# Kernel optimization log

Measured on AMD Instinct MI355X. Metric: run time of the kernel, lower is better.

## Reference

```python
import jax, jax.numpy as jnp
import numpy as np

B, N, D = 64, 128, 32
P = N * (N - 1)          # ordered pairs
H1, H2, HF = 32, 32, 16  # layer_widths=(32,32), final_widths=(16,)
EPS = 1e-5
SLOPE = 0.01             # LeakyReLU default


def _leaky(x):
    return jnp.where(x >= 0, x, SLOPE * x)


def setup_inputs() -> dict:
    key = jax.random.key(0)
    ks = jax.random.split(key, 16)
    # all ordered pairs (i, j), i != j, grouped by source i
    src = np.repeat(np.arange(N), N - 1)
    tgt = np.array([j for i in range(N) for j in range(N) if j != i])
    s = 0.1
    return {
        "inputs": jax.random.normal(ks[0], (B, N, D), jnp.float32),
        "src": jnp.asarray(src, jnp.int32),
        "tgt": jnp.asarray(tgt, jnp.int32),
        # edge MLP: Linear(2D,32) -> BN1d(P) -> LeakyReLU -> Linear(32,32) -> LeakyReLU -> Linear(32, 1+D)
        "W1": jax.random.normal(ks[1], (2 * D, H1), jnp.float32) * s,
        "b1": jnp.zeros((H1,), jnp.float32),
        "g1": jnp.ones((P,), jnp.float32),
        "be1": jnp.zeros((P,), jnp.float32),
        "W2": jax.random.normal(ks[2], (H1, H2), jnp.float32) * s,
        "b2": jnp.zeros((H2,), jnp.float32),
        "W3": jax.random.normal(ks[3], (H2, 1 + D), jnp.float32) * s,
        "b3": jnp.zeros((1 + D,), jnp.float32),
        # final MLP: Linear(2D,16) -> BN1d(16) -> LeakyReLU -> Linear(16, D)
        "Wf1": jax.random.normal(ks[4], (2 * D, HF), jnp.float32) * s,
        "bf1": jnp.zeros((HF,), jnp.float32),
        "gf": jnp.ones((HF,), jnp.float32),
        "bef": jnp.zeros((HF,), jnp.float32),
        "Wf2": jax.random.normal(ks[5], (HF, D), jnp.float32) * s,
        "bf2": jnp.zeros((D,), jnp.float32),
    }


def reference(inputs, src, tgt, W1, b1, g1, be1, W2, b2, W3, b3,
              Wf1, bf1, gf, bef, Wf2, bf2):
    b, n, d = inputs.shape
    # gather pair features: (B, P, 2D)
    paired = jnp.concatenate([inputs[:, src], inputs[:, tgt]], axis=2)
    h = paired @ W1 + b1                              # (B, P, H1)
    # BatchNorm1d(P) on (B, P, H1): normalize per pair channel over (batch, feat)
    m = h.mean(axis=(0, 2), keepdims=True)
    v = h.var(axis=(0, 2), keepdims=True)
    h = (h - m) * jax.lax.rsqrt(v + EPS) * g1[None, :, None] + be1[None, :, None]
    h = _leaky(h) @ W2 + b2
    h = _leaky(h) @ W3 + b3                           # (B, P, 1+D)
    edges = jax.nn.sigmoid(h[..., :1])                # (B, P, 1)
    messages = h[..., 1:]                             # (B, P, D)
    weighted = edges * messages
    # segment-sum over the (N-1) senders per source node
    agg = weighted.reshape(b, n, n - 1, d).sum(axis=2)  # (B, N, D)
    sm = jnp.concatenate([inputs, agg], axis=2).reshape(-1, 2 * d)
    f = sm @ Wf1 + bf1                                # (B*N, HF)
    mf = f.mean(axis=0)
    vf = f.var(axis=0)
    f = (f - mf) * jax.lax.rsqrt(vf + EPS) * gf + bef
    out = _leaky(f) @ Wf2 + bf2
    return edges[..., 0], out.reshape(b, n, d)
```

## Files before the change

kernel.cpp:

```cpp
#include <hip/hip_runtime.h>
#include <hip/hip_bf16.h>
#include <math.h>

#define BB 64
#define NN 128
#define DD 32
#define PP (NN * (NN - 1))
#define EPSF 1e-5f

typedef __attribute__((ext_vector_type(8))) short bf16x8;
typedef __attribute__((ext_vector_type(4))) float f32x4;

static __device__ __forceinline__ unsigned short f2bf(float x) {
    unsigned u = __builtin_bit_cast(unsigned, x);
    u += 0x7fff + ((u >> 16) & 1);
    return (unsigned short)(u >> 16);
}
static __device__ __forceinline__ unsigned pk2bf(float a, float b) {
    return (unsigned)f2bf(a) | ((unsigned)f2bf(b) << 16);
}
static __device__ __forceinline__ float leakyf(float x) {
    return fmaxf(x, 0.01f * x);
}

__global__ __launch_bounds__(256) void proj_kernel(
    const float* __restrict__ inputs, const float* __restrict__ W1,
    const float* __restrict__ b1,
    const float* __restrict__ W2, const float* __restrict__ W3,
    float* __restrict__ AT, float* __restrict__ BT,
    unsigned short* __restrict__ ATh, unsigned short* __restrict__ BTh,
    float* __restrict__ SA, float* __restrict__ QA,
    float* __restrict__ SB, float* __restrict__ QB,
    unsigned short* __restrict__ W2p, unsigned short* __restrict__ W3p,
    float* __restrict__ fpartA, float* __restrict__ fpartB)
{
    __shared__ float Xs[64][33];
    __shared__ float W1s[64][32];
    __shared__ float red[4][4];

    int n = blockIdx.x, tid = threadIdx.x;

    for (int idx = tid; idx < 2048; idx += 256) {
        int b = idx >> 5, d = idx & 31;
        Xs[b][d] = inputs[((size_t)b << 12) + ((size_t)n << 5) + d];
        W1s[idx >> 5][idx & 31] = W1[idx];
    }
    __syncthreads();

    int j = tid & 31, rb = tid >> 5;
    float b1j = b1[j];
    float sa = 0.f, qa = 0.f, sb = 0.f, qb = 0.f;
    #pragma unroll
    for (int i = 0; i < 8; ++i) {
        int b = rb * 8 + i;
        float a = b1j, c = 0.f;
        #pragma unroll
        for (int k = 0; k < 32; ++k) {
            a += Xs[b][k] * W1s[k][j];
            c += Xs[b][k] * W1s[32 + k][j];
        }
        size_t off = ((size_t)n * 64 + b) * 32 + j;
        AT[off] = a;  BT[off] = c;
        ATh[off] = f2bf(a);  BTh[off] = f2bf(c);
        sa += a; qa += a * a; sb += c; qb += c * c;
    }
    #pragma unroll
    for (int off = 32; off > 0; off >>= 1) {
        sa += __shfl_down(sa, off, 64);
        qa += __shfl_down(qa, off, 64);
        sb += __shfl_down(sb, off, 64);
        qb += __shfl_down(qb, off, 64);
    }
    int w = tid >> 6;
    if ((tid & 63) == 0) { red[w][0] = sa; red[w][1] = qa; red[w][2] = sb; red[w][3] = qb; }
    __syncthreads();
    if (tid == 0) {
        SA[n] = red[0][0] + red[1][0] + red[2][0] + red[3][0];
        QA[n] = red[0][1] + red[1][1] + red[2][1] + red[3][1];
        SB[n] = red[0][2] + red[1][2] + red[2][2] + red[3][2];
        QB[n] = red[0][3] + red[1][3] + red[2][3] + red[3][3];
    }

    if (blockIdx.x == 0 && tid < 64) {
        int l = tid, nn2 = l & 15, kc = l >> 4;
        #pragma unroll
        for (int ct = 0; ct < 2; ++ct)
            #pragma unroll
            for (int jj = 0; jj < 8; ++jj) {
                int k = kc * 8 + jj;
                W2p[(ct * 64 + l) * 8 + jj] = f2bf(W2[k * 32 + ct * 16 + nn2]);
            }
        #pragma unroll
        for (int ct = 0; ct < 3; ++ct)
            #pragma unroll
            for (int jj = 0; jj < 8; ++jj) {
                int k = kc * 8 + jj;
                int c = ct * 16 + nn2;
                W3p[(ct * 64 + l) * 8 + jj] = f2bf(c < 33 ? W3[k * 33 + c] : 0.f);
            }
    }
    if (blockIdx.x == 1) {
        for (int idx = tid; idx < 1024; idx += 256) {
            fpartA[idx] = 0.f;
            fpartB[idx] = 0.f;
        }
    }
}

__global__ __launch_bounds__(256) void stats2_kernel(
    const unsigned short* __restrict__ ATh, const unsigned short* __restrict__ BTh,
    const float* __restrict__ SA, const float* __restrict__ QA,
    const float* __restrict__ SB, const float* __restrict__ QB,
    const float* __restrict__ g1, const float* __restrict__ be1,
    float* __restrict__ statA, float* __restrict__ statB)
{
    __shared__ __align__(16) float part[4][64][4];
    int tid = threadIdx.x;
    int lane = tid & 63, w = tid >> 6;
    int s0 = (blockIdx.x >> 3) * 16, t0 = (blockIdx.x & 7) * 16;

    int m = lane & 15, kc = lane >> 4;
    const unsigned short* abase = ATh + (size_t)(s0 + m) * 2048 + kc * 8 + w * 512;
    const unsigned short* bbase = BTh + (size_t)(t0 + m) * 2048 + kc * 8 + w * 512;

    f32x4 acc = {0.f, 0.f, 0.f, 0.f};
    #pragma unroll
    for (int step = 0; step < 16; ++step) {
        bf16x8 av = *(const bf16x8*)(abase + step * 32);
        bf16x8 bv = *(const bf16x8*)(bbase + step * 32);
        acc = __builtin_amdgcn_mfma_f32_16x16x32_bf16(av, bv, acc, 0, 0, 0);
    }
    *(f32x4*)&part[w][lane][0] = acc;
    __syncthreads();

    if (w == 0) {
        #pragma unroll
        for (int ww = 1; ww < 4; ++ww) {
            f32x4 o = *(const f32x4*)&part[ww][lane][0];
            acc[0] += o[0]; acc[1] += o[1]; acc[2] += o[2]; acc[3] += o[3];
        }
        int col = lane & 15, quad = lane >> 4;
        int t = t0 + col;
        float sbt = SB[t], qbt = QB[t];
        #pragma unroll
        for (int r = 0; r < 4; ++r) {
            int s = s0 + quad * 4 + r;
            if (s != t) {
                int e = t - (t > s);
                int p = s * 127 + e;
                float S = SA[s] + sbt;
                float Q = QA[s] + qbt + 2.f * acc[r];
                float mean = S * (1.f / 2048.f);
                float var  = Q * (1.f / 2048.f) - mean * mean;
                float inv  = rsqrtf(var + EPSF);
                float sc   = inv * g1[p];
                statA[p] = sc;
                statB[p] = be1[p] - mean * sc;
            }
        }
    }
}

__global__ __launch_bounds__(256) void edges_kernel(
    const float* __restrict__ AT, const float* __restrict__ BT,
    const float* __restrict__ statA, const float* __restrict__ statB,
    const unsigned short* __restrict__ W2p, const unsigned short* __restrict__ W3p,
    const float* __restrict__ b2, const float* __restrict__ b3,
    const float* __restrict__ inputs, const float* __restrict__ Wf1,
    const float* __restrict__ bf1,
    float* __restrict__ edges_out, float* __restrict__ agg,
    float* __restrict__ f, float* __restrict__ fpartA, float* __restrict__ fpartB)
{
    __shared__ __align__(16) unsigned short Abuf[8][64][8];
    __shared__ __align__(16) unsigned short Hbuf[8][64][8];
    __shared__ __align__(16) float evb[128];
    __shared__ float aggbuf[32];

    int tid = threadIdx.x;
    int b = blockIdx.x >> 7;
    int s = blockIdx.x & 127;

    if (tid < 32) aggbuf[tid] = 0.f;

    int e2 = tid >> 1;
    int half = tid & 1;
    int k0 = half * 16;
    int m = e2 & 15, r = e2 >> 4;
    const float* arow = AT + ((size_t)s * 64 + b) * 32;

    float nh[16];
    if (e2 < 127) {
        int t = e2 + (e2 >= s);
        int p = s * 127 + e2;
        float sc = statA[p], sh = statB[p];
        const float4* brow = (const float4*)(BT + ((size_t)t * 64 + b) * 32 + k0);
        const float4* ar4  = (const float4*)(arow + k0);
        #pragma unroll
        for (int q = 0; q < 4; ++q) {
            float4 bv = brow[q];
            float4 av = ar4[q];
            nh[4*q+0] = leakyf((av.x + bv.x) * sc + sh);
            nh[4*q+1] = leakyf((av.y + bv.y) * sc + sh);
            nh[4*q+2] = leakyf((av.z + bv.z) * sc + sh);
            nh[4*q+3] = leakyf((av.w + bv.w) * sc + sh);
        }
    } else {
        #pragma unroll
        for (int q = 0; q < 16; ++q) nh[q] = 0.f;
    }
    union { bf16x8 v; unsigned u[4]; } U0, U1;
    #pragma unroll
    for (int q = 0; q < 4; ++q) {
        U0.u[q] = pk2bf(nh[2*q], nh[2*q+1]);
        U1.u[q] = pk2bf(nh[8+2*q], nh[8+2*q+1]);
    }
    int L0 = 2 * half * 16 + m;
    *(bf16x8*)&Abuf[r][L0][0]      = U0.v;
    *(bf16x8*)&Abuf[r][L0 + 16][0] = U1.v;

    int lane = tid & 63;
    int w = tid >> 6;
    int col = lane & 15, q4 = (lane >> 4) * 4;
    bf16x8 wb2[2], wb3[3];
    wb2[0] = *(const bf16x8*)(W2p + (0 * 64 + lane) * 8);
    wb2[1] = *(const bf16x8*)(W2p + (1 * 64 + lane) * 8);
    wb3[0] = *(const bf16x8*)(W3p + (0 * 64 + lane) * 8);
    wb3[1] = *(const bf16x8*)(W3p + (1 * 64 + lane) * 8);
    wb3[2] = *(const bf16x8*)(W3p + (2 * 64 + lane) * 8);
    float b2c0 = b2[col], b2c1 = b2[16 + col];
    float b3c[3];
    #pragma unroll
    for (int ct = 0; ct < 3; ++ct) {
        int c = ct * 16 + col;
        b3c[ct] = (c < 33) ? b3[c] : 0.f;
    }
    __syncthreads();

    #pragma unroll
    for (int rt = 0; rt < 2; ++rt) {
        int r2 = w * 2 + rt;
        bf16x8 a = *(const bf16x8*)&Abuf[r2][lane][0];
        f32x4 c0 = {0.f, 0.f, 0.f, 0.f}, c1 = {0.f, 0.f, 0.f, 0.f};
        c0 = __builtin_amdgcn_mfma_f32_16x16x32_bf16(a, wb2[0], c0, 0, 0, 0);
        c1 = __builtin_amdgcn_mfma_f32_16x16x32_bf16(a, wb2[1], c1, 0, 0, 0);
        #pragma unroll
        for (int reg = 0; reg < 4; ++reg) {
            float x = leakyf(c0[reg] + b2c0);
            int c = col;
            Hbuf[r2][(c >> 3) * 16 + q4 + reg][c & 7] = f2bf(x);
            float y = leakyf(c1[reg] + b2c1);
            int c2 = 16 + col;
            Hbuf[r2][(c2 >> 3) * 16 + q4 + reg][c2 & 7] = f2bf(y);
        }
    }
    __syncthreads();

    f32x4 o[2][3];
    #pragma unroll
    for (int rt = 0; rt < 2; ++rt) {
        int r2 = w * 2 + rt;
        bf16x8 a2 = *(const bf16x8*)&Hbuf[r2][lane][0];
        #pragma unroll
        for (int ct = 0; ct < 3; ++ct) {
            f32x4 cc = {0.f, 0.f, 0.f, 0.f};
            o[rt][ct] = __builtin_amdgcn_mfma_f32_16x16x32_bf16(a2, wb3[ct], cc, 0, 0, 0);
        }
    }

    if (col == 0) {
        #pragma unroll
        for (int rt = 0; rt < 2; ++rt) {
            int r2 = w * 2 + rt;
            int row0 = r2 * 16 + q4;
            float e0 = 1.f / (1.f + __expf(-(o[rt][0][0] + b3c[0])));
            float e1 = 1.f / (1.f + __expf(-(o[rt][0][1] + b3c[0])));
            float e2v = 1.f / (1.f + __expf(-(o[rt][0][2] + b3c[0])));
            float e3 = 1.f / (1.f + __expf(-(o[rt][0][3] + b3c[0])));
            float4 ev4;
            ev4.x = e0; ev4.y = e1; ev4.z = e2v;
            ev4.w = (row0 == 124) ? 0.f : e3;
            *(float4*)&evb[row0] = ev4;
            float* ep = edges_out + (size_t)b * PP + s * 127 + row0;
            ep[0] = e0; ep[1] = e1; ep[2] = e2v;
            if (row0 != 124) ep[3] = e3;
        }
    }
    __syncthreads();

    #pragma unroll
    for (int ct = 0; ct < 3; ++ct) {
        int c = ct * 16 + col;
        if (c >= 1 && c <= 32) {
            float part = 0.f;
            #pragma unroll
            for (int rt = 0; rt < 2; ++rt) {
                int row0 = (w * 2 + rt) * 16 + q4;
                float4 ev4 = *(const float4*)&evb[row0];
                float bb3 = b3c[ct];
                part += ev4.x * (o[rt][ct][0] + bb3);
                part += ev4.y * (o[rt][ct][1] + bb3);
                part += ev4.z * (o[rt][ct][2] + bb3);
                part += ev4.w * (o[rt][ct][3] + bb3);
            }
            atomicAdd(&aggbuf[c - 1], part);
        }
    }
    __syncthreads();

    size_t row = (size_t)b * 128 + s;
    if (tid < 32) agg[row * 32 + tid] = aggbuf[tid];

    if (tid < 16) {
        const float* xrow = inputs + row * 32;
        float acc = bf1[tid];
        #pragma unroll
        for (int k = 0; k < 32; ++k) acc += xrow[k] * Wf1[k * 16 + tid];
        #pragma unroll
        for (int k = 0; k < 32; ++k) acc += aggbuf[k] * Wf1[(32 + k) * 16 + tid];
        f[row * 16 + tid] = acc;
        int bucket = blockIdx.x & 63;
        atomicAdd(&fpartA[bucket * 16 + tid], acc);
        atomicAdd(&fpartB[bucket * 16 + tid], acc * acc);
    }
}

__global__ __launch_bounds__(256) void out_kernel(
    const float* __restrict__ f,
    const float* __restrict__ fpartA, const float* __restrict__ fpartB,
    const float* __restrict__ gf, const float* __restrict__ bef,
    const float* __restrict__ Wf2, const float* __restrict__ bf2,
    float* __restrict__ outp)
{
    __shared__ float Wf2s[16][32];
    __shared__ float sc[16], sh[16];
    __shared__ float fs[8][16];

    int tid = threadIdx.x;
    for (int idx = tid; idx < 512; idx += 256)
        Wf2s[idx >> 5][idx & 31] = Wf2[idx];
    if (tid < 16) {
        float S = 0.f, Q = 0.f;
        #pragma unroll
        for (int g = 0; g < 64; ++g) {
            S += fpartA[g * 16 + tid];
            Q += fpartB[g * 16 + tid];
        }
        float mean = S * (1.f / 8192.f);
        float var  = Q * (1.f / 8192.f) - mean * mean;
        float inv  = rsqrtf(var + EPSF);
        float s    = inv * gf[tid];
        sc[tid] = s;
        sh[tid] = bef[tid] - mean * s;
    }
    int row0 = blockIdx.x * 8;
    if (tid < 128) {
        int r = tid >> 4, j = tid & 15;
        fs[r][j] = f[(size_t)(row0 + r) * 16 + j];
    }
    __syncthreads();

    int rl = tid >> 5, d = tid & 31;
    float acc = bf2[d];
    #pragma unroll
    for (int j = 0; j < 16; ++j) {
        float v = fs[rl][j] * sc[j] + sh[j];
        v = fmaxf(v, 0.01f * v);
        acc += v * Wf2s[j][d];
    }
    outp[(size_t)(row0 + rl) * 32 + d] = acc;
}

extern "C" void kernel_launch(void* const* d_in, const int* in_sizes, int n_in,
                              void* d_out, int out_size, void* d_ws, size_t ws_size,
                              hipStream_t stream) {
    const float* inputs = (const float*)d_in[0];
    const float* W1   = (const float*)d_in[3];
    const float* b1   = (const float*)d_in[4];
    const float* g1   = (const float*)d_in[5];
    const float* be1  = (const float*)d_in[6];
    const float* W2   = (const float*)d_in[7];
    const float* b2   = (const float*)d_in[8];
    const float* W3   = (const float*)d_in[9];
    const float* b3   = (const float*)d_in[10];
    const float* Wf1  = (const float*)d_in[11];
    const float* bf1  = (const float*)d_in[12];
    const float* gf   = (const float*)d_in[13];
    const float* bef  = (const float*)d_in[14];
    const float* Wf2  = (const float*)d_in[15];
    const float* bf2  = (const float*)d_in[16];

    float* ws    = (float*)d_ws;
    float* AT    = ws;
    float* BT    = AT + 262144;
    float* SA    = BT + 262144;
    float* QA    = SA + 128;
    float* SB    = QA + 128;
    float* QB    = SB + 128;
    float* statA = QB + 128;
    float* statB = statA + PP;
    float* region = statB + PP;
    unsigned short* ATh = (unsigned short*)region;
    unsigned short* BTh = ATh + 262144;
    float* agg = region;
    float* f   = region + 262144;
    float* fpartA = region + 393216;
    float* fpartB = fpartA + 1024;
    unsigned short* W2p = (unsigned short*)(fpartB + 1024);
    unsigned short* W3p = W2p + 1024;

    float* edges_out = (float*)d_out;
    float* outp      = edges_out + (size_t)BB * PP;

    proj_kernel<<<128, 256, 0, stream>>>(inputs, W1, b1, W2, W3,
                                         AT, BT, ATh, BTh, SA, QA, SB, QB,
                                         W2p, W3p, fpartA, fpartB);
    stats2_kernel<<<64, 256, 0, stream>>>(ATh, BTh, SA, QA, SB, QB,
                                          g1, be1, statA, statB);
    edges_kernel<<<BB * NN, 256, 0, stream>>>(AT, BT, statA, statB, W2p, W3p,
                                              b2, b3, inputs, Wf1, bf1,
                                              edges_out, agg, f, fpartA, fpartB);
    out_kernel<<<8192 / 8, 256, 0, stream>>>(f, fpartA, fpartB, gf, bef, Wf2, bf2, outp);
}
```

Measured before the change: 148.6 us.

## Rebalance proj, edges and stats kernels: split proj grid, batch edges blocks, shuffle reductions

Splits the projection kernel across 4 batch quarters (512 blocks) and writes per-quarter sum/sumsq partials that stats2 combines. The stats2 MFMA chain is split into two independent accumulators to shorten its dependency chain. The edges kernel now processes 4 batch entries per block (2048 blocks), hoisting stat, weight and Wf1 loads into shared memory once per block. It also replaces shared-memory atomics and the edge-value buffer with wave shuffles and per-wave partial buffers. The trade is more serial work and more barriers per edges block and less parallelism overall.

```diff
diff --git a/kernel.cpp b/kernel.cpp
--- a/kernel.cpp
+++ b/kernel.cpp
@@ -15,9 +15,6 @@
     unsigned u = __builtin_bit_cast(unsigned, x);
     u += 0x7fff + ((u >> 16) & 1);
     return (unsigned short)(u >> 16);
-}
-static __device__ __forceinline__ unsigned pk2bf(float a, float b) {
-    return (unsigned)f2bf(a) | ((unsigned)f2bf(b) << 16);
 }
 static __device__ __forceinline__ float leakyf(float x) {
     return fmaxf(x, 0.01f * x);
@@ -29,35 +26,38 @@
     const float* __restrict__ W2, const float* __restrict__ W3,
     float* __restrict__ AT, float* __restrict__ BT,
     unsigned short* __restrict__ ATh, unsigned short* __restrict__ BTh,
-    float* __restrict__ SA, float* __restrict__ QA,
-    float* __restrict__ SB, float* __restrict__ QB,
+    float* __restrict__ SQp,
     unsigned short* __restrict__ W2p, unsigned short* __restrict__ W3p,
     float* __restrict__ fpartA, float* __restrict__ fpartB)
 {
-    __shared__ float Xs[64][33];
-    __shared__ float W1s[64][32];
-    __shared__ float red[4][4];
-
-    int n = blockIdx.x, tid = threadIdx.x;
-
-    for (int idx = tid; idx < 2048; idx += 256) {
-        int b = idx >> 5, d = idx & 31;
-        Xs[b][d] = inputs[((size_t)b << 12) + ((size_t)n << 5) + d];
-        W1s[idx >> 5][idx & 31] = W1[idx];
+    __shared__ float Xs[16 * 33];
+    __shared__ float W1s[2048];
+    __shared__ float red[16];
+
+    int tid = threadIdx.x;
+    int n = blockIdx.x >> 2, q = blockIdx.x & 3;
+
+    for (int idx = tid; idx < 2048; idx += 256) W1s[idx] = W1[idx];
+    for (int idx = tid; idx < 512; idx += 256) {
+        int r = idx >> 5, d = idx & 31;
+        Xs[r * 33 + d] = inputs[(size_t)(q * 16 + r) * 4096 + n * 32 + d];
     }
     __syncthreads();
 
     int j = tid & 31, rb = tid >> 5;
+    int lane = tid & 63, w = tid >> 6;
     float b1j = b1[j];
     float sa = 0.f, qa = 0.f, sb = 0.f, qb = 0.f;
     #pragma unroll
-    for (int i = 0; i < 8; ++i) {
-        int b = rb * 8 + i;
+    for (int i = 0; i < 2; ++i) {
+        int r = rb * 2 + i;
+        int b = q * 16 + r;
         float a = b1j, c = 0.f;
         #pragma unroll
         for (int k = 0; k < 32; ++k) {
-            a += Xs[b][k] * W1s[k][j];
-            c += Xs[b][k] * W1s[32 + k][j];
+            float x = Xs[r * 33 + k];
+            a += x * W1s[k * 32 + j];
+            c += x * W1s[(32 + k) * 32 + j];
         }
         size_t off = ((size_t)n * 64 + b) * 32 + j;
         AT[off] = a;  BT[off] = c;
@@ -65,20 +65,21 @@
         sa += a; qa += a * a; sb += c; qb += c * c;
     }
     #pragma unroll
-    for (int off = 32; off > 0; off >>= 1) {
-        sa += __shfl_down(sa, off, 64);
-        qa += __shfl_down(qa, off, 64);
-        sb += __shfl_down(sb, off, 64);
-        qb += __shfl_down(qb, off, 64);
-    }
-    int w = tid >> 6;
-    if ((tid & 63) == 0) { red[w][0] = sa; red[w][1] = qa; red[w][2] = sb; red[w][3] = qb; }
+    for (int d = 32; d > 0; d >>= 1) {
+        sa += __shfl_down(sa, d, 64);
+        qa += __shfl_down(qa, d, 64);
+        sb += __shfl_down(sb, d, 64);
+        qb += __shfl_down(qb, d, 64);
+    }
+    if (lane == 0) { red[w*4+0] = sa; red[w*4+1] = qa; red[w*4+2] = sb; red[w*4+3] = qb; }
     __syncthreads();
     if (tid == 0) {
-        SA[n] = red[0][0] + red[1][0] + red[2][0] + red[3][0];
-        QA[n] = red[0][1] + red[1][1] + red[2][1] + red[3][1];
-        SB[n] = red[0][2] + red[1][2] + red[2][2] + red[3][2];
-        QB[n] = red[0][3] + red[1][3] + red[2][3] + red[3][3];
+        float4 v;
+        v.x = red[0] + red[4] + red[8]  + red[12];
+        v.y = red[1] + red[5] + red[9]  + red[13];
+        v.z = red[2] + red[6] + red[10] + red[14];
+        v.w = red[3] + red[7] + red[11] + red[15];
+        ((float4*)SQp)[n * 4 + q] = v;
     }
 
     if (blockIdx.x == 0 && tid < 64) {
@@ -95,8 +96,8 @@
             #pragma unroll
             for (int jj = 0; jj < 8; ++jj) {
                 int k = kc * 8 + jj;
-                int c = ct * 16 + nn2;
-                W3p[(ct * 64 + l) * 8 + jj] = f2bf(c < 33 ? W3[k * 33 + c] : 0.f);
+                int c2 = ct * 16 + nn2;
+                W3p[(ct * 64 + l) * 8 + jj] = f2bf(c2 < 33 ? W3[k * 33 + c2] : 0.f);
             }
     }
     if (blockIdx.x == 1) {
@@ -109,12 +110,11 @@
 
 __global__ __launch_bounds__(256) void stats2_kernel(
     const unsigned short* __restrict__ ATh, const unsigned short* __restrict__ BTh,
-    const float* __restrict__ SA, const float* __restrict__ QA,
-    const float* __restrict__ SB, const float* __restrict__ QB,
+    const float* __restrict__ SQp,
     const float* __restrict__ g1, const float* __restrict__ be1,
     float* __restrict__ statA, float* __restrict__ statB)
 {
-    __shared__ __align__(16) float part[4][64][4];
+    __shared__ __align__(16) float part[4 * 64 * 4];
     int tid = threadIdx.x;
     int lane = tid & 63, w = tid >> 6;
     int s0 = (blockIdx.x >> 3) * 16, t0 = (blockIdx.x & 7) * 16;
@@ -123,33 +123,50 @@
     const unsigned short* abase = ATh + (size_t)(s0 + m) * 2048 + kc * 8 + w * 512;
     const unsigned short* bbase = BTh + (size_t)(t0 + m) * 2048 + kc * 8 + w * 512;
 
-    f32x4 acc = {0.f, 0.f, 0.f, 0.f};
+    f32x4 acc0 = {0.f, 0.f, 0.f, 0.f}, acc1 = {0.f, 0.f, 0.f, 0.f};
     #pragma unroll
-    for (int step = 0; step < 16; ++step) {
-        bf16x8 av = *(const bf16x8*)(abase + step * 32);
-        bf16x8 bv = *(const bf16x8*)(bbase + step * 32);
-        acc = __builtin_amdgcn_mfma_f32_16x16x32_bf16(av, bv, acc, 0, 0, 0);
-    }
-    *(f32x4*)&part[w][lane][0] = acc;
+    for (int step = 0; step < 8; ++step) {
+        bf16x8 av0 = *(const bf16x8*)(abase + (2 * step) * 32);
+        bf16x8 bv0 = *(const bf16x8*)(bbase + (2 * step) * 32);
+        acc0 = __builtin_amdgcn_mfma_f32_16x16x32_bf16(av0, bv0, acc0, 0, 0, 0);
+        bf16x8 av1 = *(const bf16x8*)(abase + (2 * step + 1) * 32);
+        bf16x8 bv1 = *(const bf16x8*)(bbase + (2 * step + 1) * 32);
+        acc1 = __builtin_amdgcn_mfma_f32_16x16x32_bf16(av1, bv1, acc1, 0, 0, 0);
+    }
+    f32x4 acc;
+    acc[0] = acc0[0] + acc1[0]; acc[1] = acc0[1] + acc1[1];
+    acc[2] = acc0[2] + acc1[2]; acc[3] = acc0[3] + acc1[3];
+    *(f32x4*)&part[(w * 64 + lane) * 4] = acc;
     __syncthreads();
 
     if (w == 0) {
         #pragma unroll
         for (int ww = 1; ww < 4; ++ww) {
-            f32x4 o = *(const f32x4*)&part[ww][lane][0];
-            acc[0] += o[0]; acc[1] += o[1]; acc[2] += o[2]; acc[3] += o[3];
+            f32x4 o2 = *(const f32x4*)&part[(ww * 64 + lane) * 4];
+            acc[0] += o2[0]; acc[1] += o2[1]; acc[2] += o2[2]; acc[3] += o2[3];
         }
         int col = lane & 15, quad = lane >> 4;
         int t = t0 + col;
-        float sbt = SB[t], qbt = QB[t];
+        float sbt = 0.f, qbt = 0.f;
+        #pragma unroll
+        for (int o2 = 0; o2 < 4; ++o2) {
+            float4 v = ((const float4*)SQp)[t * 4 + o2];
+            sbt += v.z; qbt += v.w;
+        }
         #pragma unroll
         for (int r = 0; r < 4; ++r) {
             int s = s0 + quad * 4 + r;
             if (s != t) {
+                float sas = 0.f, qas = 0.f;
+                #pragma unroll
+                for (int o2 = 0; o2 < 4; ++o2) {
+                    float4 v = ((const float4*)SQp)[s * 4 + o2];
+                    sas += v.x; qas += v.y;
+                }
                 int e = t - (t > s);
                 int p = s * 127 + e;
-                float S = SA[s] + sbt;
-                float Q = QA[s] + qbt + 2.f * acc[r];
+                float S = sas + sbt;
+                float Q = qas + qbt + 2.f * acc[r];
                 float mean = S * (1.f / 2048.f);
                 float var  = Q * (1.f / 2048.f) - mean * mean;
                 float inv  = rsqrtf(var + EPSF);
@@ -168,59 +185,34 @@
     const float* __restrict__ b2, const float* __restrict__ b3,
     const float* __restrict__ inputs, const float* __restrict__ Wf1,
     const float* __restrict__ bf1,
-    float* __restrict__ edges_out, float* __restrict__ agg,
+    float* __restrict__ edges_out,
     float* __restrict__ f, float* __restrict__ fpartA, float* __restrict__ fpartB)
 {
-    __shared__ __align__(16) unsigned short Abuf[8][64][8];
-    __shared__ __align__(16) unsigned short Hbuf[8][64][8];
-    __shared__ __align__(16) float evb[128];
-    __shared__ float aggbuf[32];
+    __shared__ __align__(16) unsigned short Abuf[4096];
+    __shared__ __align__(16) unsigned short Hbuf[4096];
+    __shared__ float Wf1s[1024];
+    __shared__ float aggbuf[4][32];
 
     int tid = threadIdx.x;
-    int b = blockIdx.x >> 7;
     int s = blockIdx.x & 127;
-
-    if (tid < 32) aggbuf[tid] = 0.f;
+    int o = blockIdx.x >> 7;
+    int lane = tid & 63, w = tid >> 6;
+
+    for (int idx = tid; idx < 1024; idx += 256) Wf1s[idx] = Wf1[idx];
 
     int e2 = tid >> 1;
     int half = tid & 1;
     int k0 = half * 16;
     int m = e2 & 15, r = e2 >> 4;
-    const float* arow = AT + ((size_t)s * 64 + b) * 32;
-
-    float nh[16];
-    if (e2 < 127) {
-        int t = e2 + (e2 >= s);
-        int p = s * 127 + e2;
-        float sc = statA[p], sh = statB[p];
-        const float4* brow = (const float4*)(BT + ((size_t)t * 64 + b) * 32 + k0);
-        const float4* ar4  = (const float4*)(arow + k0);
-        #pragma unroll
-        for (int q = 0; q < 4; ++q) {
-            float4 bv = brow[q];
-            float4 av = ar4[q];
-            nh[4*q+0] = leakyf((av.x + bv.x) * sc + sh);
-            nh[4*q+1] = leakyf((av.y + bv.y) * sc + sh);
-            nh[4*q+2] = leakyf((av.z + bv.z) * sc + sh);
-            nh[4*q+3] = leakyf((av.w + bv.w) * sc + sh);
-        }
-    } else {
-        #pragma unroll
-        for (int q = 0; q < 16; ++q) nh[q] = 0.f;
-    }
-    union { bf16x8 v; unsigned u[4]; } U0, U1;
-    #pragma unroll
-    for (int q = 0; q < 4; ++q) {
-        U0.u[q] = pk2bf(nh[2*q], nh[2*q+1]);
-        U1.u[q] = pk2bf(nh[8+2*q], nh[8+2*q+1]);
-    }
     int L0 = 2 * half * 16 + m;
-    *(bf16x8*)&Abuf[r][L0][0]      = U0.v;
-    *(bf16x8*)&Abuf[r][L0 + 16][0] = U1.v;
-
-    int lane = tid & 63;
-    int w = tid >> 6;
+    bool valid = (e2 < 127);
+    int t = valid ? (e2 + (e2 >= s)) : 0;
+    int pe = s * 127 + (valid ? e2 : 126);
+    float sc = 0.f, sh = 0.f;
+    if (valid) { sc = statA[pe]; sh = statB[pe]; }
+
     int col = lane & 15, q4 = (lane >> 4) * 4;
+    int qbase = lane & 48;
     bf16x8 wb2[2], wb3[3];
     wb2[0] = *(const bf16x8*)(W2p + (0 * 64 + lane) * 8);
     wb2[1] = *(const bf16x8*)(W2p + (1 * 64 + lane) * 8);
@@ -234,93 +226,127 @@
         int c = ct * 16 + col;
         b3c[ct] = (c < 33) ? b3[c] : 0.f;
     }
-    __syncthreads();
-
-    #pragma unroll
-    for (int rt = 0; rt < 2; ++rt) {
-        int r2 = w * 2 + rt;
-        bf16x8 a = *(const bf16x8*)&Abuf[r2][lane][0];
-        f32x4 c0 = {0.f, 0.f, 0.f, 0.f}, c1 = {0.f, 0.f, 0.f, 0.f};
-        c0 = __builtin_amdgcn_mfma_f32_16x16x32_bf16(a, wb2[0], c0, 0, 0, 0);
-        c1 = __builtin_amdgcn_mfma_f32_16x16x32_bf16(a, wb2[1], c1, 0, 0, 0);
-        #pragma unroll
-        for (int reg = 0; reg < 4; ++reg) {
-            float x = leakyf(c0[reg] + b2c0);
-            int c = col;
-            Hbuf[r2][(c >> 3) * 16 + q4 + reg][c & 7] = f2bf(x);
-            float y = leakyf(c1[reg] + b2c1);
-            int c2 = 16 + col;
-            Hbuf[r2][(c2 >> 3) * 16 + q4 + reg][c2 & 7] = f2bf(y);
-        }
-    }
-    __syncthreads();
-
-    f32x4 o[2][3];
-    #pragma unroll
-    for (int rt = 0; rt < 2; ++rt) {
-        int r2 = w * 2 + rt;
-        bf16x8 a2 = *(const bf16x8*)&Hbuf[r2][lane][0];
-        #pragma unroll
-        for (int ct = 0; ct < 3; ++ct) {
-            f32x4 cc = {0.f, 0.f, 0.f, 0.f};
-            o[rt][ct] = __builtin_amdgcn_mfma_f32_16x16x32_bf16(a2, wb3[ct], cc, 0, 0, 0);
-        }
-    }
-
-    if (col == 0) {
+
+    for (int bi = 0; bi < 4; ++bi) {
+        int b = o * 4 + bi;
+        __syncthreads();
+
+        float nh[16];
+        if (valid) {
+            const float4* brow = (const float4*)(BT + ((size_t)t * 64 + b) * 32 + k0);
+            const float4* ar4  = (const float4*)(AT + ((size_t)s * 64 + b) * 32 + k0);
+            #pragma unroll
+            for (int q = 0; q < 4; ++q) {
+                float4 bv = brow[q];
+                float4 av = ar4[q];
+                nh[4*q+0] = leakyf((av.x + bv.x) * sc + sh);
+                nh[4*q+1] = leakyf((av.y + bv.y) * sc + sh);
+                nh[4*q+2] = leakyf((av.z + bv.z) * sc + sh);
+                nh[4*q+3] = leakyf((av.w + bv.w) * sc + sh);
+            }
+        } else {
+            #pragma unroll
+            for (int q = 0; q < 16; ++q) nh[q] = 0.f;
+        }
+        bf16x8 v0, v1;
+        #pragma unroll
+        for (int jj = 0; jj < 8; ++jj) {
+            v0[jj] = (short)f2bf(nh[jj]);
+            v1[jj] = (short)f2bf(nh[8 + jj]);
+        }
+        *(bf16x8*)&Abuf[((size_t)r * 64 + L0) * 8]      = v0;
+        *(bf16x8*)&Abuf[((size_t)r * 64 + L0 + 16) * 8] = v1;
+        __syncthreads();
+
         #pragma unroll
         for (int rt = 0; rt < 2; ++rt) {
             int r2 = w * 2 + rt;
-            int row0 = r2 * 16 + q4;
-            float e0 = 1.f / (1.f + __expf(-(o[rt][0][0] + b3c[0])));
-            float e1 = 1.f / (1.f + __expf(-(o[rt][0][1] + b3c[0])));
-            float e2v = 1.f / (1.f + __expf(-(o[rt][0][2] + b3c[0])));
-            float e3 = 1.f / (1.f + __expf(-(o[rt][0][3] + b3c[0])));
-            float4 ev4;
-            ev4.x = e0; ev4.y = e1; ev4.z = e2v;
-            ev4.w = (row0 == 124) ? 0.f : e3;
-            *(float4*)&evb[row0] = ev4;
-            float* ep = edges_out + (size_t)b * PP + s * 127 + row0;
-            ep[0] = e0; ep[1] = e1; ep[2] = e2v;
-            if (row0 != 124) ep[3] = e3;
-        }
-    }
-    __syncthreads();
-
-    #pragma unroll
-    for (int ct = 0; ct < 3; ++ct) {
-        int c = ct * 16 + col;
-        if (c >= 1 && c <= 32) {
-            float part = 0.f;
-            #pragma unroll
-            for (int rt = 0; rt < 2; ++rt) {
-                int row0 = (w * 2 + rt) * 16 + q4;
-                float4 ev4 = *(const float4*)&evb[row0];
-                float bb3 = b3c[ct];
-                part += ev4.x * (o[rt][ct][0] + bb3);
-                part += ev4.y * (o[rt][ct][1] + bb3);
-                part += ev4.z * (o[rt][ct][2] + bb3);
-                part += ev4.w * (o[rt][ct][3] + bb3);
-            }
-            atomicAdd(&aggbuf[c - 1], part);
-        }
-    }
-    __syncthreads();
-
-    size_t row = (size_t)b * 128 + s;
-    if (tid < 32) agg[row * 32 + tid] = aggbuf[tid];
-
-    if (tid < 16) {
-        const float* xrow = inputs + row * 32;
-        float acc = bf1[tid];
-        #pragma unroll
-        for (int k = 0; k < 32; ++k) acc += xrow[k] * Wf1[k * 16 + tid];
-        #pragma unroll
-        for (int k = 0; k < 32; ++k) acc += aggbuf[k] * Wf1[(32 + k) * 16 + tid];
-        f[row * 16 + tid] = acc;
-        int bucket = blockIdx.x & 63;
-        atomicAdd(&fpartA[bucket * 16 + tid], acc);
-        atomicAdd(&fpartB[bucket * 16 + tid], acc * acc);
+            bf16x8 a = *(const bf16x8*)&Abuf[((size_t)r2 * 64 + lane) * 8];
+            f32x4 c0 = {0.f, 0.f, 0.f, 0.f}, c1 = {0.f, 0.f, 0.f, 0.f};
+            c0 = __builtin_amdgcn_mfma_f32_16x16x32_bf16(a, wb2[0], c0, 0, 0, 0);
+            c1 = __builtin_amdgcn_mfma_f32_16x16x32_bf16(a, wb2[1], c1, 0, 0, 0);
+            #pragma unroll
+            for (int reg = 0; reg < 4; ++reg) {
+                float x = leakyf(c0[reg] + b2c0);
+                int c = col;
+                Hbuf[((size_t)r2 * 64 + (c >> 3) * 16 + q4 + reg) * 8 + (c & 7)] = f2bf(x);
+                float y = leakyf(c1[reg] + b2c1);
+                int c2 = 16 + col;
+                Hbuf[((size_t)r2 * 64 + (c2 >> 3) * 16 + q4 + reg) * 8 + (c2 & 7)] = f2bf(y);
+            }
+        }
+        __syncthreads();
+
+        f32x4 oo[2][3];
+        #pragma unroll
+        for (int rt = 0; rt < 2; ++rt) {
+            int r2 = w * 2 + rt;
+            bf16x8 a2 = *(const bf16x8*)&Hbuf[((size_t)r2 * 64 + lane) * 8];
+            #pragma unroll
+            for (int ct = 0; ct < 3; ++ct) {
+                f32x4 cc = {0.f, 0.f, 0.f, 0.f};
+                oo[rt][ct] = __builtin_amdgcn_mfma_f32_16x16x32_bf16(a2, wb3[ct], cc, 0, 0, 0);
+            }
+        }
+
+        float ev[2][4];
+        #pragma unroll
+        for (int rt = 0; rt < 2; ++rt) {
+            int row0 = (w * 2 + rt) * 16 + q4;
+            float e0 = 0.f, e1 = 0.f, e2v = 0.f, e3 = 0.f;
+            if (col == 0) {
+                e0  = 1.f / (1.f + __expf(-(oo[rt][0][0] + b3c[0])));
+                e1  = 1.f / (1.f + __expf(-(oo[rt][0][1] + b3c[0])));
+                e2v = 1.f / (1.f + __expf(-(oo[rt][0][2] + b3c[0])));
+                e3  = 1.f / (1.f + __expf(-(oo[rt][0][3] + b3c[0])));
+                float* ep = edges_out + (size_t)b * PP + s * 127 + row0;
+                ep[0] = e0; ep[1] = e1; ep[2] = e2v;
+                if (row0 != 124) ep[3] = e3;
+            }
+            ev[rt][0] = __shfl(e0,  qbase, 64);
+            ev[rt][1] = __shfl(e1,  qbase, 64);
+            ev[rt][2] = __shfl(e2v, qbase, 64);
+            ev[rt][3] = __shfl(e3,  qbase, 64);
+            if (row0 == 124) ev[rt][3] = 0.f;
+        }
+
+        #pragma unroll
+        for (int ct = 0; ct < 3; ++ct) {
+            int c = ct * 16 + col;
+            if (c >= 1 && c <= 32) {
+                float part = 0.f;
+                #pragma unroll
+                for (int rt = 0; rt < 2; ++rt) {
+                    float bb3 = b3c[ct];
+                    part += ev[rt][0] * (oo[rt][ct][0] + bb3);
+                    part += ev[rt][1] * (oo[rt][ct][1] + bb3);
+                    part += ev[rt][2] * (oo[rt][ct][2] + bb3);
+                    part += ev[rt][3] * (oo[rt][ct][3] + bb3);
+                }
+                part += __shfl_xor(part, 16, 64);
+                part += __shfl_xor(part, 32, 64);
+                if ((lane >> 4) == 0) aggbuf[w][c - 1] = part;
+            }
+        }
+        __syncthreads();
+
+        size_t row = (size_t)b * 128 + s;
+        if (tid < 32) {
+            float tot = aggbuf[0][tid] + aggbuf[1][tid] + aggbuf[2][tid] + aggbuf[3][tid];
+            aggbuf[0][tid] = tot;
+        }
+        if (tid < 16) {
+            const float* xrow = inputs + row * 32;
+            float acc = bf1[tid];
+            #pragma unroll
+            for (int k = 0; k < 32; ++k) acc += xrow[k] * Wf1s[k * 16 + tid];
+            #pragma unroll
+            for (int k = 0; k < 32; ++k) acc += aggbuf[0][k] * Wf1s[(32 + k) * 16 + tid];
+            f[row * 16 + tid] = acc;
+            int bucket = ((blockIdx.x << 2) + bi) & 63;
+            atomicAdd(&fpartA[bucket * 16 + tid], acc);
+            atomicAdd(&fpartB[bucket * 16 + tid], acc * acc);
+        }
     }
 }
 
@@ -331,13 +357,12 @@
     const float* __restrict__ Wf2, const float* __restrict__ bf2,
     float* __restrict__ outp)
 {
-    __shared__ float Wf2s[16][32];
+    __shared__ float Wf2s[512];
     __shared__ float sc[16], sh[16];
-    __shared__ float fs[8][16];
+    __shared__ float fs[128];
 
     int tid = threadIdx.x;
-    for (int idx = tid; idx < 512; idx += 256)
-        Wf2s[idx >> 5][idx & 31] = Wf2[idx];
+    for (int idx = tid; idx < 512; idx += 256) Wf2s[idx] = Wf2[idx];
     if (tid < 16) {
         float S = 0.f, Q = 0.f;
         #pragma unroll
@@ -348,14 +373,14 @@
         float mean = S * (1.f / 8192.f);
         float var  = Q * (1.f / 8192.f) - mean * mean;
         float inv  = rsqrtf(var + EPSF);
-        float s    = inv * gf[tid];
-        sc[tid] = s;
-        sh[tid] = bef[tid] - mean * s;
+        float s2   = inv * gf[tid];
+        sc[tid] = s2;
+        sh[tid] = bef[tid] - mean * s2;
     }
     int row0 = blockIdx.x * 8;
     if (tid < 128) {
         int r = tid >> 4, j = tid & 15;
-        fs[r][j] = f[(size_t)(row0 + r) * 16 + j];
+        fs[r * 16 + j] = f[(size_t)(row0 + r) * 16 + j];
     }
     __syncthreads();
 
@@ -363,9 +388,9 @@
     float acc = bf2[d];
     #pragma unroll
     for (int j = 0; j < 16; ++j) {
-        float v = fs[rl][j] * sc[j] + sh[j];
-        v = fmaxf(v, 0.01f * v);
-        acc += v * Wf2s[j][d];
+        float v = fs[rl * 16 + j] * sc[j] + sh[j];
+        v = leakyf(v);
+        acc += v * Wf2s[j * 32 + d];
     }
     outp[(size_t)(row0 + rl) * 32 + d] = acc;
 }
@@ -389,35 +414,29 @@
     const float* Wf2  = (const float*)d_in[15];
     const float* bf2  = (const float*)d_in[16];
 
-    float* ws    = (float*)d_ws;
-    float* AT    = ws;
-    float* BT    = AT + 262144;
-    float* SA    = BT + 262144;
-    float* QA    = SA + 128;
-    float* SB    = QA + 128;
-    float* QB    = SB + 128;
-    float* statA = QB + 128;
-    float* statB = statA + PP;
-    float* region = statB + PP;
-    unsigned short* ATh = (unsigned short*)region;
+    float* ws = (float*)d_ws;
+    float* AT     = ws;
+    float* BT     = ws + 262144;
+    unsigned short* ATh = (unsigned short*)(ws + 524288);
     unsigned short* BTh = ATh + 262144;
-    float* agg = region;
-    float* f   = region + 262144;
-    float* fpartA = region + 393216;
-    float* fpartB = fpartA + 1024;
-    unsigned short* W2p = (unsigned short*)(fpartB + 1024);
+    float* SQp    = ws + 786432;
+    float* statA  = ws + 790528;
+    float* statB  = ws + 806784;
+    float* f      = ws + 823040;
+    float* fpartA = ws + 954112;
+    float* fpartB = ws + 955136;
+    unsigned short* W2p = (unsigned short*)(ws + 956160);
     unsigned short* W3p = W2p + 1024;
 
     float* edges_out = (float*)d_out;
     float* outp      = edges_out + (size_t)BB * PP;
 
-    proj_kernel<<<128, 256, 0, stream>>>(inputs, W1, b1, W2, W3,
-                                         AT, BT, ATh, BTh, SA, QA, SB, QB,
+    proj_kernel<<<512, 256, 0, stream>>>(inputs, W1, b1, W2, W3,
+                                         AT, BT, ATh, BTh, SQp,
                                          W2p, W3p, fpartA, fpartB);
-    stats2_kernel<<<64, 256, 0, stream>>>(ATh, BTh, SA, QA, SB, QB,
-                                          g1, be1, statA, statB);
-    edges_kernel<<<BB * NN, 256, 0, stream>>>(AT, BT, statA, statB, W2p, W3p,
-                                              b2, b3, inputs, Wf1, bf1,
-                                              edges_out, agg, f, fpartA, fpartB);
-    out_kernel<<<8192 / 8, 256, 0, stream>>>(f, fpartA, fpartB, gf, bef, Wf2, bf2, outp);
-}
+    stats2_kernel<<<64, 256, 0, stream>>>(ATh, BTh, SQp, g1, be1, statA, statB);
+    edges_kernel<<<2048, 256, 0, stream>>>(AT, BT, statA, statB, W2p, W3p,
+                                           b2, b3, inputs, Wf1, bf1,
+                                           edges_out, f, fpartA, fpartB);
+    out_kernel<<<1024, 256, 0, stream>>>(f, fpartA, fpartB, gf, bef, Wf2, bf2, outp);
+}
```

Measured after the change: 145.3 us. 2.2% less time.
